# Kernel tuning notes

Measured on AMD Instinct MI355X. Metric: run time of the kernel, lower is better.

The kernel has to match this reference:

```python
import jax, jax.numpy as jnp
import numpy as np

NUM_HEADS = 8
HEAD_DIM = 96  # dim_out // num_heads = 768 // 8
DIM_OUT = 768
STRIDE = 2


def setup_inputs() -> dict:
    key = jax.random.key(0)
    k1, k2, k3, k4, k5 = jax.random.split(key, 5)
    B, H, W, C = 4, 64, 64, 384
    hidden_states = jax.random.normal(k1, (B, H, W, C), dtype=jnp.float32)
    qkv_w = jax.random.normal(k2, (C, 3 * DIM_OUT), dtype=jnp.float32) * (C ** -0.5)
    qkv_b = jax.random.normal(k3, (3 * DIM_OUT,), dtype=jnp.float32) * 0.02
    proj_w = jax.random.normal(k4, (DIM_OUT, DIM_OUT), dtype=jnp.float32) * (DIM_OUT ** -0.5)
    proj_b = jax.random.normal(k5, (DIM_OUT,), dtype=jnp.float32) * 0.02
    return {"hidden_states": hidden_states, "qkv_w": qkv_w, "qkv_b": qkv_b,
            "proj_w": proj_w, "proj_b": proj_b}


def reference(hidden_states, qkv_w, qkv_b, proj_w, proj_b):
    B, H, W, C = hidden_states.shape
    scale = HEAD_DIM ** -0.5
    # QKV projection over channels
    qkv = jnp.einsum('bhwc,cd->bhwd', hidden_states, qkv_w) + qkv_b  # [B,H,W,3*Do]
    qkv = qkv.reshape(B, H * W, 3, NUM_HEADS, HEAD_DIM)
    q, k, v = qkv[:, :, 0], qkv[:, :, 1], qkv[:, :, 2]  # [B, HW, nh, hd]
    # Max-pool queries spatially by STRIDE
    q = q.reshape(B, H, W, DIM_OUT)
    Hq, Wq = H // STRIDE, W // STRIDE
    q = q.reshape(B, Hq, STRIDE, Wq, STRIDE, DIM_OUT).max(axis=(2, 4))  # [B,Hq,Wq,Do]
    q = q.reshape(B, Hq * Wq, NUM_HEADS, HEAD_DIM)
    # Attention: Lq = Hq*Wq, Lk = H*W
    attn = jnp.einsum('bqhd,bkhd->bhqk', q * scale, k)
    attn = jax.nn.softmax(attn, axis=-1)
    out = jnp.einsum('bhqk,bkhd->bqhd', attn, v)  # [B,Lq,nh,hd]
    out = out.reshape(B, Hq, Wq, DIM_OUT)
    out = jnp.einsum('bhwc,cd->bhwd', out, proj_w) + proj_b
    return out
```

## Files before the change

### kernel.cpp

```cpp
#include <hip/hip_runtime.h>
#include <hip/hip_bf16.h>

typedef unsigned short u16;
typedef __attribute__((ext_vector_type(8))) short bf16x8;
typedef __attribute__((ext_vector_type(8))) unsigned short u16x8;
typedef __attribute__((ext_vector_type(4))) float f32x4;

#define MFMA16(a,b,c) __builtin_amdgcn_mfma_f32_16x16x32_bf16(a,b,c,0,0,0)

__device__ __forceinline__ u16 f2bf(float f) {
  union { float f; unsigned int u; } v; v.f = f;
  unsigned int r = v.u + 0x7fffu + ((v.u >> 16) & 1u);
  return (u16)(r >> 16);
}
__device__ __forceinline__ float bf2f(u16 u) {
  union { unsigned int i; float f; } v; v.i = ((unsigned int)u) << 16; return v.f;
}
__device__ __forceinline__ float exp2a(float x) {
  float r;
  asm("v_exp_f32 %0, %1" : "=v"(r) : "v"(x));
  return r;
}
__device__ __forceinline__ float max3(float a, float b, float c) {
  float r;
  asm("v_max3_f32 %0, %1, %2, %3" : "=v"(r) : "v"(a), "v"(b), "v"(c));
  return r;
}

__device__ __forceinline__ void gld16(const void* g, void* l) {
  __builtin_amdgcn_global_load_lds((const __attribute__((address_space(1))) void*)g,
                                   (__attribute__((address_space(3))) void*)l, 16, 0, 0);
}

__device__ __forceinline__ void ttrans_body(const float* __restrict__ in, u16* __restrict__ out,
                                            int K, int N, int blk, int tid, u16 T[64][65]) {
  const int ntx = N >> 6;
  const int tx = blk % ntx, ty = blk / ntx;
  const int n0 = tx * 64, k0 = ty * 64;
  #pragma unroll
  for (int p = 0; p < 4; ++p) {
    int idx = p * 256 + tid;
    int r = idx >> 4, ch = idx & 15;
    float4 v = *reinterpret_cast<const float4*>(in + (size_t)(k0 + r) * N + n0 + ch * 4);
    T[r][ch * 4 + 0] = f2bf(v.x);
    T[r][ch * 4 + 1] = f2bf(v.y);
    T[r][ch * 4 + 2] = f2bf(v.z);
    T[r][ch * 4 + 3] = f2bf(v.w);
  }
  __syncthreads();
  #pragma unroll
  for (int p = 0; p < 2; ++p) {
    int idx = p * 256 + tid;
    int rr = idx >> 3, ch = idx & 7;
    u16x8 o;
    #pragma unroll
    for (int e = 0; e < 8; ++e) o[e] = T[ch * 8 + e][rr];
    *reinterpret_cast<u16x8*>(out + (size_t)(n0 + rr) * K + k0 + ch * 8) = o;
  }
}

__global__ void prep(const float* __restrict__ hs, u16* __restrict__ hs_bf,
                     const float* __restrict__ qkv_w, u16* __restrict__ qkvwT,
                     const float* __restrict__ proj_w, u16* __restrict__ projwT) {
  __shared__ u16 T[64][65];
  const int blk = blockIdx.x, tid = threadIdx.x;
  if (blk < 6144) {
    int i = blk * 256 + tid;
    float4 v = reinterpret_cast<const float4*>(hs)[i];
    ushort4 o; o.x = f2bf(v.x); o.y = f2bf(v.y); o.z = f2bf(v.z); o.w = f2bf(v.w);
    reinterpret_cast<ushort4*>(hs_bf)[i] = o;
  } else if (blk < 6360) {
    ttrans_body(qkv_w, qkvwT, 384, 2304, blk - 6144, tid, T);
  } else {
    ttrans_body(proj_w, projwT, 768, 768, blk - 6360, tid, T);
  }
}

template<int EPI, int MT>
__launch_bounds__(256)
__global__ void gemm_bt(const u16* __restrict__ A, const u16* __restrict__ Bt,
                        const float* __restrict__ bias,
                        u16* __restrict__ qp, u16* __restrict__ ok, u16* __restrict__ ov,
                        float* __restrict__ of, int K, int nbx, int cpx) {
  constexpr int ASZ = MT * 32;
  constexpr int MI = MT / 32;
  __shared__ __align__(16) u16 Sh[2 * ASZ + 8192];
  const int id = blockIdx.x;
  const int id2 = (id & 7) * cpx + (id >> 3);
  const int bx = id2 % nbx, by = id2 / nbx;
  const int tid = threadIdx.x;
  const int wave = tid >> 6, lane = tid & 63;
  const int c = lane & 15, g = lane >> 4;
  const int brow = by * MT, bcol = bx * 128;
  const int wr = (wave >> 1) * (MT / 2), wc = (wave & 1) * 64;
  f32x4 acc[MI][4] = {};
  const int srow = (MT == 128) ? (wave * 32 + (lane >> 2)) : (wave * 16 + (lane >> 2));
  const int scol = (lane & 3) * 8;
  const u16* agp0 = A  + (size_t)(brow + srow) * K + scol;
  const u16* agp1 = A  + (size_t)(brow + srow + 16) * K + scol;
  const int bsrow = wave * 32 + (lane >> 2);
  const u16* bgp0 = Bt + (size_t)(bcol + bsrow) * K + scol;
  const u16* bgp1 = Bt + (size_t)(bcol + bsrow + 16) * K + scol;
  const int alo = (MT == 128) ? (wave * 1024) : (wave * 512);
  const int blo = 2 * ASZ + wave * 1024;
  const int nk = K >> 5;
  gld16(agp0, &Sh[alo]);
  if (MT == 128) gld16(agp1, &Sh[alo + 512]);
  gld16(bgp0, &Sh[blo]);
  gld16(bgp1, &Sh[blo + 512]);
  for (int ks = 0; ks < nk; ++ks) {
    const int cur = ks & 1;
    if (ks + 1 < nk) {
      const int k1 = (ks + 1) << 5;
      const int anb = (cur ^ 1) * ASZ;
      const int bnb = (cur ^ 1) * 4096;
      gld16(agp0 + k1, &Sh[anb + alo]);
      if (MT == 128) gld16(agp1 + k1, &Sh[anb + alo + 512]);
      gld16(bgp0 + k1, &Sh[blo + bnb]);
      gld16(bgp1 + k1, &Sh[blo + bnb + 512]);
      if (MT == 128) { asm volatile("s_waitcnt vmcnt(4)" ::: "memory"); }
      else           { asm volatile("s_waitcnt vmcnt(3)" ::: "memory"); }
    } else {
      asm volatile("s_waitcnt vmcnt(0)" ::: "memory");
    }
    __builtin_amdgcn_s_barrier();
    __builtin_amdgcn_sched_barrier(0);
    const int acb = cur * ASZ;
    const int bcb = 2 * ASZ + cur * 4096;
    bf16x8 af[MI], bfr[4];
    #pragma unroll
    for (int mi = 0; mi < MI; ++mi)
      af[mi] = *reinterpret_cast<const bf16x8*>(&Sh[acb + (wr + mi * 16 + c) * 32 + g * 8]);
    #pragma unroll
    for (int ni = 0; ni < 4; ++ni)
      bfr[ni] = *reinterpret_cast<const bf16x8*>(&Sh[bcb + (wc + ni * 16 + c) * 32 + g * 8]);
    #pragma unroll
    for (int mi = 0; mi < MI; ++mi)
      #pragma unroll
      for (int ni = 0; ni < 4; ++ni)
        acc[mi][ni] = MFMA16(af[mi], bfr[ni], acc[mi][ni]);
    __builtin_amdgcn_sched_barrier(0);
    __builtin_amdgcn_s_barrier();
  }
  if (EPI == 0 && MT == 128 && bcol < 768) {
    const float SC = 0.14724744f;
    float* P = (float*)&Sh[0];
    float m01[4][4], m23[4][4];
    #pragma unroll
    for (int mi = 0; mi < MI; ++mi)
      #pragma unroll
      for (int ni = 0; ni < 4; ++ni) {
        m01[mi][ni] = fmaxf(acc[mi][ni][0], acc[mi][ni][1]);
        m23[mi][ni] = fmaxf(acc[mi][ni][2], acc[mi][ni][3]);
      }
    if (wr == 64) {
      #pragma unroll
      for (int mi = 0; mi < MI; ++mi)
        #pragma unroll
        for (int ni = 0; ni < 4; ++ni) {
          const int pw = mi * 8 + g * 2;
          P[(wave & 1) * 2048 + pw * 64 + ni * 16 + c]       = m01[mi][ni];
          P[(wave & 1) * 2048 + (pw + 1) * 64 + ni * 16 + c] = m23[mi][ni];
        }
    }
    __syncthreads();
    if (wr == 0) {
      const int b = brow >> 12;
      const int hq = (brow >> 7) & 31;
      const size_t rbase = (size_t)(b * 1024 + hq * 32);
      #pragma unroll
      for (int mi = 0; mi < MI; ++mi)
        #pragma unroll
        for (int ni = 0; ni < 4; ++ni) {
          const int col = bcol + wc + ni * 16 + c;
          const float bz = bias[col];
          const int pw = mi * 8 + g * 2;
          float v0 = fmaxf(m01[mi][ni], P[(wave & 1) * 2048 + pw * 64 + ni * 16 + c]);
          float v1 = fmaxf(m23[mi][ni], P[(wave & 1) * 2048 + (pw + 1) * 64 + ni * 16 + c]);
          qp[(rbase + pw) * 768 + col]     = f2bf((v0 + bz) * SC);
          qp[(rbase + pw + 1) * 768 + col] = f2bf((v1 + bz) * SC);
        }
    }
    return;
  }
  if (EPI == 0 && MT == 128 && bcol >= 1536) {
    u16* T = &Sh[0];
    const int vc0 = bcol - 1536;
    const int bq = brow >> 12;
    const int s0 = brow & 4095;
    #pragma unroll
    for (int ni = 0; ni < 4; ++ni) {
      const int j = wc + ni * 16 + c;
      const float bz = bias[bcol + j];
      const int key = (j & 15) << 2;
      #pragma unroll
      for (int mi = 0; mi < MI; ++mi) {
        const int rb = wr + mi * 16 + g * 4;
        ushort4 o;
        o.x = f2bf(acc[mi][ni][0] + bz);
        o.y = f2bf(acc[mi][ni][1] + bz);
        o.z = f2bf(acc[mi][ni][2] + bz);
        o.w = f2bf(acc[mi][ni][3] + bz);
        *reinterpret_cast<ushort4*>(&T[j * 128 + (rb ^ key)]) = o;
      }
    }
    __syncthreads();
    u16* vb2 = ov + ((size_t)(bq * 768 + vc0)) * 4096 + s0;
    #pragma unroll
    for (int p = 0; p < 8; ++p) {
      const int j = p * 16 + wave * 4 + (lane >> 4);
      const int sc = lane & 15;
      const int key = j & 15;
      const int p4 = 8 * (sc >> 3) + 2 * (sc & 3) + ((sc >> 2) & 1);
      uint2 lo = *reinterpret_cast<uint2*>(&T[j * 128 + ((sc ^ key) << 2)]);
      uint2 hi = *reinterpret_cast<uint2*>(&T[j * 128 + (((sc + 16) ^ key) << 2)]);
      *reinterpret_cast<uint2*>(vb2 + (size_t)j * 4096 + p4 * 4)      = lo;
      *reinterpret_cast<uint2*>(vb2 + (size_t)j * 4096 + 64 + p4 * 4) = hi;
    }
    return;
  }
  #pragma unroll
  for (int mi = 0; mi < MI; ++mi) {
    #pragma unroll
    for (int ni = 0; ni < 4; ++ni) {
      const int col = bcol + wc + ni * 16 + c;
      const float bz = bias[col];
      #pragma unroll
      for (int i = 0; i < 4; ++i) {
        const int row = brow + wr + mi * 16 + g * 4 + i;
        float v = acc[mi][ni][i] + bz;
        if (EPI == 0) {
          ok[(size_t)row * 768 + col - 768] = f2bf(v);
        } else {
          of[(size_t)row * 768 + col] = v;
        }
      }
    }
  }
}

__launch_bounds__(512, 4)
__global__ void flash8(const u16* __restrict__ Qp, const u16* __restrict__ Kb,
                       const u16* __restrict__ Vtg, u16* __restrict__ aout) {
  const int blk = blockIdx.x;
  const int xcd = blk & 7, j = blk >> 3;
  const int bh = xcd + 8 * (j >> 4), qt = j & 15;
  const int b = bh >> 3, h = bh & 7;
  __shared__ __align__(16) u16 Sh[24576];
  const int tid = threadIdx.x, w = tid >> 6, lane = tid & 63;
  const int sq = w >> 2, wq = w & 3;
  const int c = lane & 15, g = lane >> 4;
  const int kbase = sq * 12288;
  const int vbase = 6144 + sq * 12288;
  const u16* qb = Qp + ((size_t)(b * 1024 + qt * 64 + wq * 16 + c)) * 768 + h * 96;
  bf16x8 qf[3];
  #pragma unroll
  for (int kc = 0; kc < 3; ++kc)
    qf[kc] = *reinterpret_cast<const bf16x8*>(qb + kc * 32 + g * 8);
  const u16* kp[3];
  const u16* vp[3];
  int loff[3];
  {
    const u16* kb0 = Kb + ((size_t)(b * 4096 + sq * 2048)) * 768 + h * 96;
    const u16* vb0 = Vtg + ((size_t)(bh * 96)) * 4096 + sq * 2048;
    #pragma unroll
    for (int j2 = 0; j2 < 3; ++j2) {
      int p = wq * 192 + j2 * 64 + lane;
      int r = p / 12, ch = p - r * 12;
      kp[j2] = kb0 + r * 768 + ch * 8;
      int d = p >> 3, vch = p & 7;
      vp[j2] = vb0 + d * 4096 + ((vch ^ (d & 7)) * 8);
      loff[j2] = (wq * 192 + j2 * 64) * 8;
    }
  }
  float m = -1e30f, l = 0.f;
  f32x4 acc[6] = {};
  const f32x4 z4 = {0.f, 0.f, 0.f, 0.f};
  const int sw = (c & 7) << 3;
  for (int kt = 0; kt < 32; ++kt) {
    __syncthreads();
    #pragma unroll
    for (int j2 = 0; j2 < 3; ++j2) gld16(kp[j2], &Sh[kbase + loff[j2]]);
    #pragma unroll
    for (int j2 = 0; j2 < 3; ++j2) gld16(vp[j2], &Sh[vbase + loff[j2]]);
    #pragma unroll
    for (int j2 = 0; j2 < 3; ++j2) { kp[j2] += 49152; vp[j2] += 64; }
    __syncthreads();
    f32x4 st[4];
    __builtin_amdgcn_s_setprio(1);
    #pragma unroll
    for (int kt4 = 0; kt4 < 4; ++kt4) {
      bf16x8 kf = *reinterpret_cast<const bf16x8*>(&Sh[kbase + (kt4 * 16 + c) * 96 + g * 8]);
      st[kt4] = MFMA16(kf, qf[0], z4);
    }
    #pragma unroll
    for (int kc = 1; kc < 3; ++kc)
      #pragma unroll
      for (int kt4 = 0; kt4 < 4; ++kt4) {
        bf16x8 kf = *reinterpret_cast<const bf16x8*>(&Sh[kbase + (kt4 * 16 + c) * 96 + kc * 32 + g * 8]);
        st[kt4] = MFMA16(kf, qf[kc], st[kt4]);
      }
    __builtin_amdgcn_s_setprio(0);
    float pmax;
    {
      float a0 = max3(st[0][0], st[0][1], st[0][2]);
      float a1 = max3(st[0][3], st[1][0], st[1][1]);
      float a2 = max3(st[1][2], st[1][3], st[2][0]);
      float a3 = max3(st[2][1], st[2][2], st[2][3]);
      float a4 = max3(st[3][0], st[3][1], st[3][2]);
      pmax = fmaxf(max3(a0, a1, st[3][3]), max3(a2, a3, a4));
    }
    pmax = fmaxf(pmax, __shfl_xor(pmax, 16));
    pmax = fmaxf(pmax, __shfl_xor(pmax, 32));
    if (__any(pmax > m + 8.0f)) {
      float mn = fmaxf(m, pmax);
      float esc = exp2a(m - mn);
      m = mn;
      l *= esc;
      float er[4];
      #pragma unroll
      for (int i = 0; i < 4; ++i) er[i] = __shfl(esc, g * 4 + i);
      #pragma unroll
      for (int dc = 0; dc < 6; ++dc)
        #pragma unroll
        for (int i = 0; i < 4; ++i)
          acc[dc][i] *= er[i];
    }
    float ps = 0.f;
    #pragma unroll
    for (int kt4 = 0; kt4 < 4; ++kt4)
      #pragma unroll
      for (int i = 0; i < 4; ++i) {
        float p = exp2a(st[kt4][i] - m);
        st[kt4][i] = p;
        ps += p;
      }
    ps += __shfl_xor(ps, 16);
    ps += __shfl_xor(ps, 32);
    l += ps;
    unsigned int uu[4][2];
    #pragma unroll
    for (int kt4 = 0; kt4 < 4; ++kt4) {
      asm("v_cvt_pk_bf16_f32 %0, %1, %2" : "=v"(uu[kt4][0]) : "v"(st[kt4][0]), "v"(st[kt4][1]));
      asm("v_cvt_pk_bf16_f32 %0, %1, %2" : "=v"(uu[kt4][1]) : "v"(st[kt4][2]), "v"(st[kt4][3]));
    }
    __builtin_amdgcn_s_setprio(1);
    #pragma unroll
    for (int kh = 0; kh < 2; ++kh) {
      union { unsigned int wrd[4]; bf16x8 v; } pfu;
      pfu.wrd[0] = uu[2 * kh][0];
      pfu.wrd[1] = uu[2 * kh][1];
      pfu.wrd[2] = uu[2 * kh + 1][0];
      pfu.wrd[3] = uu[2 * kh + 1][1];
      bf16x8 pf = pfu.v;
      #pragma unroll
      for (int dc = 0; dc < 6; ++dc) {
        bf16x8 vf = *reinterpret_cast<const bf16x8*>(&Sh[vbase + (dc * 16 + c) * 64 + ((kh * 32 + g * 8) ^ sw)]);
        acc[dc] = MFMA16(pf, vf, acc[dc]);
      }
    }
    __builtin_amdgcn_s_setprio(0);
  }
  __syncthreads();
  float* Cb = (float*)&Sh[0];
  float* Ml = (float*)&Sh[12288];
  if (sq == 1) {
    #pragma unroll
    for (int dc = 0; dc < 6; ++dc)
      #pragma unroll
      for (int i = 0; i < 4; ++i)
        Cb[(wq * 16 + g * 4 + i) * 96 + dc * 16 + c] = acc[dc][i];
    if (lane < 16) {
      Ml[(wq * 16 + lane) * 2]     = m;
      Ml[(wq * 16 + lane) * 2 + 1] = l;
    }
  }
  __syncthreads();
  if (sq == 0) {
    u16* ob = aout + (size_t)(b * 1024 + qt * 64 + wq * 16) * 768 + h * 96;
    #pragma unroll
    for (int i = 0; i < 4; ++i) {
      const int q = g * 4 + i;
      float m0q = __shfl(m, q), l0q = __shfl(l, q);
      float m1q = Ml[(wq * 16 + q) * 2], l1q = Ml[(wq * 16 + q) * 2 + 1];
      float M = fmaxf(m0q, m1q);
      float e0 = exp2a(m0q - M), e1 = exp2a(m1q - M);
      float inv = 1.f / (l0q * e0 + l1q * e1);
      #pragma unroll
      for (int dc = 0; dc < 6; ++dc) {
        float a1 = Cb[(wq * 16 + q) * 96 + dc * 16 + c];
        ob[(size_t)q * 768 + dc * 16 + c] = f2bf((acc[dc][i] * e0 + a1 * e1) * inv);
      }
    }
  }
}

extern "C" void kernel_launch(void* const* d_in, const int* in_sizes, int n_in,
                              void* d_out, int out_size, void* d_ws, size_t ws_size,
                              hipStream_t stream) {
  const float* hs     = (const float*)d_in[0];
  const float* qkv_w  = (const float*)d_in[1];
  const float* qkv_b  = (const float*)d_in[2];
  const float* proj_w = (const float*)d_in[3];
  const float* proj_b = (const float*)d_in[4];
  float* out = (float*)d_out;

  u16* hs_bf  = (u16*)d_ws;
  u16* qkvwT  = hs_bf  + 6291456;
  u16* projwT = qkvwT  + 884736;
  u16* vT     = projwT + 589824;
  u16* kbuf   = vT     + 12582912;
  u16* spare  = kbuf   + 12582912;
  u16* qpol   = spare  + 12582912;
  u16* aout   = qpol   + 3145728;

  prep<<<6504, 256, 0, stream>>>(hs, hs_bf, qkv_w, qkvwT, proj_w, projwT);

  gemm_bt<0, 128><<<2304, 256, 0, stream>>>(hs_bf, qkvwT, qkv_b,
                                            qpol, kbuf, vT, nullptr, 384, 18, 288);
  flash8<<<512, 512, 0, stream>>>(qpol, kbuf, vT, aout);
  gemm_bt<1, 64><<<384, 256, 0, stream>>>(aout, projwT, proj_b,
                                          nullptr, nullptr, nullptr, out, 768, 6, 48);
}
```

Before: 144.8 us.

## Double-buffer K tiles and overlap V load with QK compute in flash kernel

The attention kernel now keeps two K tile buffers in shared memory and prefetches the next K tile while the current one is consumed. The V load for the current step is issued before the QK^T MFMAs and waited on separately with vmcnt counters, so the V fetch overlaps the score computation and softmax. Shared memory per block grows from 48KB to 72KB, which may reduce occupancy, and an extra barrier per iteration is added.

Result: slower. 149.5 us (+3.2%).

```diff
diff --git a/kernel.cpp b/kernel.cpp
--- a/kernel.cpp
+++ b/kernel.cpp
@@ -240,18 +240,18 @@
 }
 
 __launch_bounds__(512, 4)
-__global__ void flash8(const u16* __restrict__ Qp, const u16* __restrict__ Kb,
-                       const u16* __restrict__ Vtg, u16* __restrict__ aout) {
+__global__ void flash11(const u16* __restrict__ Qp, const u16* __restrict__ Kb,
+                        const u16* __restrict__ Vtg, u16* __restrict__ aout) {
   const int blk = blockIdx.x;
   const int xcd = blk & 7, j = blk >> 3;
   const int bh = xcd + 8 * (j >> 4), qt = j & 15;
   const int b = bh >> 3, h = bh & 7;
-  __shared__ __align__(16) u16 Sh[24576];
+  __shared__ __align__(16) u16 Sh[36864];
   const int tid = threadIdx.x, w = tid >> 6, lane = tid & 63;
   const int sq = w >> 2, wq = w & 3;
   const int c = lane & 15, g = lane >> 4;
-  const int kbase = sq * 12288;
-  const int vbase = 6144 + sq * 12288;
+  const int sbase = sq * 18432;
+  const int vbase = sbase + 12288;
   const u16* qb = Qp + ((size_t)(b * 1024 + qt * 64 + wq * 16 + c)) * 768 + h * 96;
   bf16x8 qf[3];
   #pragma unroll
@@ -273,31 +273,40 @@
       loff[j2] = (wq * 192 + j2 * 64) * 8;
     }
   }
+  asm volatile("s_waitcnt vmcnt(0)" ::: "memory");
+  #pragma unroll
+  for (int j2 = 0; j2 < 3; ++j2) gld16(kp[j2], &Sh[sbase + loff[j2]]);
+  #pragma unroll
+  for (int j2 = 0; j2 < 3; ++j2) kp[j2] += 49152;
   float m = -1e30f, l = 0.f;
   f32x4 acc[6] = {};
   const f32x4 z4 = {0.f, 0.f, 0.f, 0.f};
   const int sw = (c & 7) << 3;
   for (int kt = 0; kt < 32; ++kt) {
-    __syncthreads();
-    #pragma unroll
-    for (int j2 = 0; j2 < 3; ++j2) gld16(kp[j2], &Sh[kbase + loff[j2]]);
+    const int cur = kt & 1;
     #pragma unroll
     for (int j2 = 0; j2 < 3; ++j2) gld16(vp[j2], &Sh[vbase + loff[j2]]);
     #pragma unroll
-    for (int j2 = 0; j2 < 3; ++j2) { kp[j2] += 49152; vp[j2] += 64; }
-    __syncthreads();
+    for (int j2 = 0; j2 < 3; ++j2) gld16(kp[j2], &Sh[sbase + (cur ^ 1) * 6144 + loff[j2]]);
+    #pragma unroll
+    for (int j2 = 0; j2 < 3; ++j2) { vp[j2] += 64; kp[j2] += 49152; }
+    __builtin_amdgcn_sched_barrier(0);
+    asm volatile("s_waitcnt vmcnt(6)" ::: "memory");
+    __builtin_amdgcn_s_barrier();
+    __builtin_amdgcn_sched_barrier(0);
+    const int kb2 = sbase + cur * 6144;
     f32x4 st[4];
     __builtin_amdgcn_s_setprio(1);
     #pragma unroll
     for (int kt4 = 0; kt4 < 4; ++kt4) {
-      bf16x8 kf = *reinterpret_cast<const bf16x8*>(&Sh[kbase + (kt4 * 16 + c) * 96 + g * 8]);
+      bf16x8 kf = *reinterpret_cast<const bf16x8*>(&Sh[kb2 + (kt4 * 16 + c) * 96 + g * 8]);
       st[kt4] = MFMA16(kf, qf[0], z4);
     }
     #pragma unroll
     for (int kc = 1; kc < 3; ++kc)
       #pragma unroll
       for (int kt4 = 0; kt4 < 4; ++kt4) {
-        bf16x8 kf = *reinterpret_cast<const bf16x8*>(&Sh[kbase + (kt4 * 16 + c) * 96 + kc * 32 + g * 8]);
+        bf16x8 kf = *reinterpret_cast<const bf16x8*>(&Sh[kb2 + (kt4 * 16 + c) * 96 + kc * 32 + g * 8]);
         st[kt4] = MFMA16(kf, qf[kc], st[kt4]);
       }
     __builtin_amdgcn_s_setprio(0);
@@ -344,6 +353,10 @@
       asm("v_cvt_pk_bf16_f32 %0, %1, %2" : "=v"(uu[kt4][0]) : "v"(st[kt4][0]), "v"(st[kt4][1]));
       asm("v_cvt_pk_bf16_f32 %0, %1, %2" : "=v"(uu[kt4][1]) : "v"(st[kt4][2]), "v"(st[kt4][3]));
     }
+    __builtin_amdgcn_sched_barrier(0);
+    asm volatile("s_waitcnt vmcnt(3)" ::: "memory");
+    __builtin_amdgcn_s_barrier();
+    __builtin_amdgcn_sched_barrier(0);
     __builtin_amdgcn_s_setprio(1);
     #pragma unroll
     for (int kh = 0; kh < 2; ++kh) {
@@ -360,6 +373,8 @@
       }
     }
     __builtin_amdgcn_s_setprio(0);
+    __builtin_amdgcn_sched_barrier(0);
+    __builtin_amdgcn_s_barrier();
   }
   __syncthreads();
   float* Cb = (float*)&Sh[0];
@@ -418,7 +433,7 @@
 
   gemm_bt<0, 128><<<2304, 256, 0, stream>>>(hs_bf, qkvwT, qkv_b,
                                             qpol, kbuf, vT, nullptr, 384, 18, 288);
-  flash8<<<512, 512, 0, stream>>>(qpol, kbuf, vT, aout);
+  flash11<<<512, 512, 0, stream>>>(qpol, kbuf, vT, aout);
   gemm_bt<1, 64><<<384, 256, 0, stream>>>(aout, projwT, proj_b,
                                           nullptr, nullptr, nullptr, out, 768, 6, 48);
 }
```
